# Optimization experiments

Measured on AMD Instinct MI355X. Metric: run time of the kernel, lower is better.

## Reference

```python
import jax, jax.numpy as jnp
import numpy as np

B, F, Q, CHUNK = 2, 8192, 4096, 512
NUM_VERTS = 6000


def _safe_div(n, d):
    return n / jnp.where(d == 0, 1.0, d)


def _bary(a, b, c, p):
    """Barycentric coords of the closest point on triangle (a,b,c) to p.
    All args broadcastable [..., 3]; returns [..., 3] (u, v, w) with
    closest = u*a + v*b + w*c. Ericson, Real-Time Collision Detection."""
    ab = b - a; ac = c - a; ap = p - a
    d1 = jnp.sum(ab * ap, -1); d2 = jnp.sum(ac * ap, -1)
    bp = p - b
    d3 = jnp.sum(ab * bp, -1); d4 = jnp.sum(ac * bp, -1)
    cp_ = p - c
    d5 = jnp.sum(ab * cp_, -1); d6 = jnp.sum(ac * cp_, -1)
    vc = d1 * d4 - d3 * d2
    vb = d5 * d2 - d1 * d6
    va = d3 * d6 - d5 * d4
    v_ab = _safe_div(d1, d1 - d3)
    w_ac = _safe_div(d2, d2 - d6)
    w_bc = _safe_div(d4 - d3, (d4 - d3) + (d5 - d6))
    inv = _safe_div(1.0, va + vb + vc)
    v_in = vb * inv; w_in = vc * inv
    zero = jnp.zeros_like(d1); one = jnp.ones_like(d1)
    conds = [(d1 <= 0) & (d2 <= 0),
             (d3 >= 0) & (d4 <= d3),
             (vc <= 0) & (d1 >= 0) & (d3 <= 0),
             (d6 >= 0) & (d5 <= d6),
             (vb <= 0) & (d2 >= 0) & (d6 <= 0),
             (va <= 0) & (d4 >= d3) & (d5 >= d6)]
    u = jnp.select(conds, [one, zero, 1 - v_ab, zero, 1 - w_ac, zero], 1 - v_in - w_in)
    v = jnp.select(conds, [zero, one, v_ab, zero, zero, 1 - w_bc], v_in)
    w = jnp.select(conds, [zero, zero, zero, one, w_ac, w_bc], w_in)
    return jnp.stack([u, v, w], -1)


def _closest_faces(triangles, points, chunk=CHUNK):
    """Exact closest-triangle index per query point (replaces BVH search).
    triangles [B,F,3,3], points [B,Q,3] -> int32 [B,Q]."""
    tri = jax.lax.stop_gradient(triangles)
    pts = jax.lax.stop_gradient(points)
    bsz, nq = pts.shape[0], pts.shape[1]
    a = tri[:, :, 0]; b = tri[:, :, 1]; c = tri[:, :, 2]  # [B,F,3]

    def one_chunk(p_chunk):  # [B,CH,3]
        pa = p_chunk[:, :, None, :]                       # [B,CH,1,3]
        bc = _bary(a[:, None], b[:, None], c[:, None], pa)  # [B,CH,F,3]
        cp = (bc[..., 0:1] * a[:, None] + bc[..., 1:2] * b[:, None]
              + bc[..., 2:3] * c[:, None])                # [B,CH,F,3]
        d2 = jnp.sum((cp - pa) ** 2, -1)                  # [B,CH,F]
        return jnp.argmin(d2, axis=-1)                    # [B,CH]

    chunks = jnp.moveaxis(pts.reshape(bsz, nq // chunk, chunk, 3), 1, 0)
    idx = jax.lax.map(one_chunk, chunks)                  # [NC,B,CH]
    return jnp.moveaxis(idx, 0, 1).reshape(bsz, nq)


def setup_inputs() -> dict:
    key = jax.random.key(0)
    k1, k2, k3, k4, k5 = jax.random.split(key, 5)
    return {
        'triangles': jax.random.normal(k1, (B, F, 3, 3), dtype=jnp.float32),
        'points': jax.random.normal(k2, (B, Q, 3), dtype=jnp.float32),
        'normals': jax.random.normal(k3, (B, F, 3, 3), dtype=jnp.float32),
        'cmaps': jax.random.normal(k4, (B, F, 3, 3), dtype=jnp.float32),
        'faces': jax.random.randint(k5, (B, F, 3), 0, NUM_VERTS, dtype=jnp.int32),
    }


def reference(triangles, points, normals, cmaps, faces):
    closest_faces = _closest_faces(triangles, points)     # [B,Q]
    idx = closest_faces[:, :, None, None]
    tri_g = jnp.take_along_axis(triangles, idx, axis=1)   # [B,Q,3,3]
    nrm_g = jnp.take_along_axis(normals, idx, axis=1)
    cmp_g = jnp.take_along_axis(cmaps, idx, axis=1)
    bcs = _bary(tri_g[:, :, 0], tri_g[:, :, 1], tri_g[:, :, 2], points)  # [B,Q,3]
    bcs = jnp.clip(bcs, 0.0, 1.0)
    closest_points = jnp.einsum('bqk,bqkd->bqd', bcs, tri_g)
    closest_normals = jnp.einsum('bqk,bqkd->bqd', bcs, nrm_g)
    closest_cmaps = jnp.einsum('bqk,bqkd->bqd', bcs, cmp_g)
    residual = closest_points - points
    closest_fids = jnp.take_along_axis(faces, closest_faces[:, :, None], axis=1)  # [B,Q,3]
    closest_idx = jnp.take_along_axis(
        closest_fids, jnp.argmax(bcs, -1)[:, :, None], axis=2)[..., 0]            # [B,Q]
    return residual, closest_normals, closest_cmaps, closest_idx
```

## Files before the change

### kernel.cpp

```cpp
#include <hip/hip_runtime.h>
#include <float.h>

#define B_   2
#define F_   8192
#define Q_   4096
#define NC   128
#define FC   (F_/NC)
#define PTS  512
#define PPT  2

typedef float f4u __attribute__((ext_vector_type(4), aligned(4)));
typedef float f2u __attribute__((ext_vector_type(2), aligned(8)));
typedef unsigned int uint;

__device__ __forceinline__ void bary_uvw(
    float ax, float ay, float az,
    float bx, float by, float bz,
    float cx, float cy, float cz,
    float px, float py, float pz,
    float& u, float& v, float& w)
{
#pragma clang fp contract(off)
    float abx = bx - ax, aby = by - ay, abz = bz - az;
    float acx = cx - ax, acy = cy - ay, acz = cz - az;
    float apx = px - ax, apy = py - ay, apz = pz - az;
    float d1 = abx*apx + aby*apy + abz*apz;
    float d2 = acx*apx + acy*apy + acz*apz;
    float bpx = px - bx, bpy = py - by, bpz = pz - bz;
    float d3 = abx*bpx + aby*bpy + abz*bpz;
    float d4 = acx*bpx + acy*bpy + acz*bpz;
    float qx = px - cx, qy = py - cy, qz = pz - cz;
    float d5 = abx*qx + aby*qy + abz*qz;
    float d6 = acx*qx + acy*qy + acz*qz;
    float vc = d1*d4 - d3*d2;
    float vb = d5*d2 - d1*d6;
    float va = d3*d6 - d5*d4;

    bool c1 = (d1 <= 0.f) && (d2 <= 0.f);
    bool c2 = (d3 >= 0.f) && (d4 <= d3);
    bool c3 = (vc <= 0.f) && (d1 >= 0.f) && (d3 <= 0.f);
    bool c4 = (d6 >= 0.f) && (d5 <= d6);
    bool c5 = (vb <= 0.f) && (d2 >= 0.f) && (d6 <= 0.f);
    bool c6 = (va <= 0.f) && (d4 >= d3) && (d5 >= d6);

    bool e1 = c1;
    bool p1 = !c1;
    bool e2 = p1 && c2;
    bool p2 = p1 && !c2;
    bool e3 = p2 && c3;
    bool p3 = p2 && !c3;
    bool e4 = p3 && c4;
    bool p4 = p3 && !c4;
    bool e5 = p4 && c5;
    bool p5 = p4 && !c5;
    bool e6 = p5 && c6;

    float d43 = d4 - d3;
    float d56 = d5 - d6;
    float n  = e3 ? d1        : (e5 ? d2        : (e6 ? d43         : 1.f));
    float dd = e3 ? (d1 - d3) : (e5 ? (d2 - d6) : (e6 ? (d43 + d56) : (va + vb + vc)));
    dd = (dd == 0.f) ? 1.f : dd;
    float t = n / dd;

    float vi = vb * t;
    float wi = vc * t;
    u = e1 ? 1.f : (e2 ? 0.f : (e3 ? 1.f - t : (e4 ? 0.f : (e5 ? 1.f - t : (e6 ? 0.f     : 1.f - vi - wi)))));
    v = e1 ? 0.f : (e2 ? 1.f : (e3 ? t       : (e4 ? 0.f : (e5 ? 0.f     : (e6 ? 1.f - t : vi)))));
    w = e1 ? 0.f : (e2 ? 0.f : (e3 ? 0.f     : (e4 ? 1.f : (e5 ? t       : (e6 ? t       : wi)))));
}

__global__ void precompute_kernel(const float* __restrict__ tri,
                                  float4* __restrict__ cons)
{
    int i = blockIdx.x * blockDim.x + threadIdx.x;
    if (i >= B_ * F_) return;
    const float* g = tri + (size_t)i * 9;
    float ax = g[0], ay = g[1], az = g[2];
    float bx = g[3], by = g[4], bz = g[5];
    float cx = g[6], cy = g[7], cz = g[8];
    float abx = bx - ax, aby = by - ay, abz = bz - az;
    float acx = cx - ax, acy = cy - ay, acz = cz - az;
    float daa = abx*abx + aby*aby + abz*abz;
    float dcc = acx*acx + acy*acy + acz*acz;
    float dac = abx*acx + aby*acy + abz*acz;
    float dbc = daa + dcc - 2.f*dac;
    float nn  = daa*dcc - dac*dac;
    float4* o = cons + (size_t)i * 6;
    o[0] = make_float4(abx, aby, abz, -(abx*ax + aby*ay + abz*az));
    o[1] = make_float4(acx, acy, acz, -(acx*ax + acy*ay + acz*az));
    o[2] = make_float4(-2.f*ax, -2.f*ay, -2.f*az, ax*ax + ay*ay + az*az);
    o[3] = make_float4(daa, dcc, -dac, nn);
    o[4] = make_float4(1.f/daa, 1.f/dcc, 1.f/dbc, 1.f/nn);
    o[5] = make_float4(daa - dac, -daa, -dcc, -dbc);
}

__device__ __forceinline__ void eval_key(
    float px, float py, float pz, float pp,
    const f4u C0, const f4u C1, const f4u C2, const f4u C3, const f4u C4,
    const f4u C5, int flv, int im, int& K0, int& K1)
{
    float d1, d2, ap, ins, sg, t1, t2, ts;
    asm("v_mov_b32 %[d1], %[nabA]\n\t"
        "v_mov_b32 %[d2], %[nacA]\n\t"
        "v_mov_b32 %[ap], %[aa]\n\t"
        "v_fmac_f32 %[d1], %[abx], %[px]\n\t"
        "v_fmac_f32 %[d2], %[acx], %[px]\n\t"
        "v_fmac_f32 %[ap], %[n2ax], %[px]\n\t"
        "v_fmac_f32 %[d1], %[aby], %[py]\n\t"
        "v_fmac_f32 %[d2], %[acy], %[py]\n\t"
        "v_fmac_f32 %[ap], %[n2ay], %[py]\n\t"
        "v_fmac_f32 %[d1], %[abz], %[pz]\n\t"
        "v_fmac_f32 %[d2], %[acz], %[pz]\n\t"
        "v_fmac_f32 %[ap], %[n2az], %[pz]\n\t"
        "v_mul_f32 %[t1], %[dcc], %[d1]\n\t"
        "v_mul_f32 %[t2], %[daa], %[d2]\n\t"
        "v_add_f32 %[ap], %[pp], %[ap]\n\t"
        "v_fmac_f32 %[t1], %[ndac], %[d2]\n\t"
        "v_fmac_f32 %[t2], %[ndac], %[d1]\n\t"
        "v_add_f32 %[ts], %[t1], %[t2]\n\t"
        "v_mul_f32 %[sg], %[d1], %[t1]\n\t"
        "v_sub_f32 %[ts], %[nn], %[ts]\n\t"
        "v_fmac_f32 %[sg], %[d2], %[t2]\n\t"
        "v_min3_f32 %[ins], %[t1], %[t2], %[ts]\n\t"
        "v_mul_f32 %[sg], %[rnn], %[sg]"
        : [d1]"=&v"(d1), [d2]"=&v"(d2), [ap]"=&v"(ap), [ins]"=&v"(ins),
          [sg]"=&v"(sg), [t1]"=&v"(t1), [t2]"=&v"(t2), [ts]"=&v"(ts)
        : [px]"v"(px), [py]"v"(py), [pz]"v"(pz), [pp]"v"(pp),
          [abx]"s"(C0.x), [aby]"s"(C0.y), [abz]"s"(C0.z), [nabA]"s"(C0.w),
          [acx]"s"(C1.x), [acy]"s"(C1.y), [acz]"s"(C1.z), [nacA]"s"(C1.w),
          [n2ax]"s"(C2.x), [n2ay]"s"(C2.y), [n2az]"s"(C2.z), [aa]"s"(C2.w),
          [daa]"s"(C3.x), [dcc]"s"(C3.y), [ndac]"s"(C3.z), [nn]"s"(C3.w),
          [rnn]"s"(C4.w));

    float ta, tc, t3, t4, t5, t7, t8;
    unsigned long long mk;
    asm("v_mul_f32 %[ta], %[rdaa], %[d1]\n\t"
        "v_mul_f32 %[tc], %[rdcc], %[d2]\n\t"
        "v_sub_f32 %[t7], %[d2], %[d1]\n\t"
        "v_med3_f32 %[ta], %[ta], 0, 1.0\n\t"
        "v_med3_f32 %[tc], %[tc], 0, 1.0\n\t"
        "v_add_f32 %[t7], %[kk], %[t7]\n\t"
        "v_add_f32 %[t3], %[d1], %[d1]\n\t"
        "v_add_f32 %[t4], %[d2], %[d2]\n\t"
        "v_mul_f32 %[t8], %[rdbc], %[t7]\n\t"
        "v_fma_f32 %[t5], %[ndaa], %[ta], %[t3]\n\t"
        "v_fma_f32 %[t4], %[ndcc], %[tc], %[t4]\n\t"
        "v_med3_f32 %[t8], %[t8], 0, 1.0\n\t"
        "v_add_f32 %[t7], %[t7], %[t7]\n\t"
        "v_mul_f32 %[ta], %[ta], %[t5]\n\t"
        "v_mul_f32 %[tc], %[tc], %[t4]\n\t"
        "v_fma_f32 %[t7], %[ndbc], %[t8], %[t7]\n\t"
        "v_subrev_f32 %[t3], %[daa], %[t3]\n\t"
        "v_mul_f32 %[t7], %[t8], %[t7]\n\t"
        "v_cmp_le_f32 %[mk], 0, %[ins]\n\t"
        "v_add_f32 %[t7], %[t3], %[t7]\n\t"
        "v_max3_f32 %[t3], %[ta], %[tc], %[t7]\n\t"
        "v_cndmask_b32 %[t3], %[t3], %[sg], %[mk]\n\t"
        "v_sub_f32 %[t4], %[ap], %[t3]\n\t"
        "v_and_or_b32 %[t4], %[t4], %[im], %[flv]\n\t"
        "v_max_i32 %[t8], %[K0], %[t4]\n\t"
        "v_min_i32 %[K0], %[K0], %[t4]\n\t"
        "v_min_i32 %[K1], %[K1], %[t8]"
        : [K0]"+v"(K0), [K1]"+v"(K1),
          [ta]"=&v"(ta), [tc]"=&v"(tc), [t3]"=&v"(t3), [t4]"=&v"(t4),
          [t5]"=&v"(t5), [t7]"=&v"(t7), [t8]"=&v"(t8), [mk]"=&s"(mk)
        : [d1]"v"(d1), [d2]"v"(d2), [ins]"v"(ins), [sg]"v"(sg), [ap]"v"(ap),
          [daa]"s"(C3.x), [rdaa]"s"(C4.x), [rdcc]"s"(C4.y), [rdbc]"s"(C4.z),
          [kk]"s"(C5.x), [ndaa]"s"(C5.y), [ndcc]"s"(C5.z), [ndbc]"s"(C5.w),
          [im]"s"(im), [flv]"v"(flv));
}

__global__ __launch_bounds__(PTS, 8) void scan_kernel(
    const float* __restrict__ tri, const float* __restrict__ pts,
    const f4u* __restrict__ cons, uint2* __restrict__ keys)
{
    const int im = ~(FC - 1);
    const int tid = threadIdx.x;
    const int pb = blockIdx.x, cb = blockIdx.y, bb = blockIdx.z;

    const int q0 = pb * (PTS * PPT) + tid * PPT;
    const float* p0 = pts + ((size_t)bb * Q_ + q0) * 3;
    f2u m0 = *(const f2u*)(p0);
    f2u m1 = *(const f2u*)(p0 + 2);
    f2u m2 = *(const f2u*)(p0 + 4);
    float px0 = m0.x, py0 = m0.y, pz0 = m1.x;
    float px1 = m1.y, py1 = m2.x, pz1 = m2.y;
    float pp0 = px0*px0 + py0*py0 + pz0*pz0;
    float pp1 = px1*px1 + py1*py1 + pz1*pz1;

    const f4u* ct = cons + ((size_t)bb * F_ + (size_t)cb * FC) * 6;

    int K00 = 0x7FFFFFFF, K01 = 0x7FFFFFFF;
    int K10 = 0x7FFFFFFF, K11 = 0x7FFFFFFF;

    f4u A0 = ct[0], A1 = ct[1], A2 = ct[2], A3 = ct[3], A4 = ct[4], A5 = ct[5];
    #pragma unroll 2
    for (int fl = 0; fl < FC; ++fl) {
        int nf = (fl + 1 < FC) ? fl + 1 : FC - 1;
        const f4u* nt = ct + nf * 6;
        f4u N0 = nt[0], N1 = nt[1], N2 = nt[2], N3 = nt[3], N4 = nt[4], N5 = nt[5];
        eval_key(px0, py0, pz0, pp0, A0, A1, A2, A3, A4, A5, fl, im, K00, K01);
        eval_key(px1, py1, pz1, pp1, A0, A1, A2, A3, A4, A5, fl, im, K10, K11);
        A0 = N0; A1 = N1; A2 = N2; A3 = N3; A4 = N4; A5 = N5;
    }

    float pxs[2] = {px0, px1};
    float pys[2] = {py0, py1};
    float pzs[2] = {pz0, pz1};
    int kk0[2] = {K00, K10};
    int kk1[2] = {K01, K11};

    #pragma unroll
    for (int p = 0; p < 2; ++p) {
        float px = pxs[p], py = pys[p], pz = pzs[p];
        float dbest = FLT_MAX; int fbest = 0x7FFFFFFF;
        #pragma unroll
        for (int j = 0; j < 2; ++j) {
            int lf = (j == 0 ? kk0[p] : kk1[p]) & (FC - 1);
            const float* tg = tri + ((size_t)bb * F_ + (size_t)cb * FC + lf) * 9;
            f4u ra4 = *(const f4u*)(tg);
            f4u rb4 = *(const f4u*)(tg + 4);
            float rc8 = tg[8];
            float u, v, w;
            bary_uvw(ra4.x, ra4.y, ra4.z, ra4.w, rb4.x, rb4.y,
                     rb4.z, rb4.w, rc8, px, py, pz, u, v, w);
            float d2v;
            {
#pragma clang fp contract(off)
                float cpx = u*ra4.x + v*ra4.w + w*rb4.z;
                float cpy = u*ra4.y + v*rb4.x + w*rb4.w;
                float cpz = u*ra4.z + v*rb4.y + w*rc8;
                float dx = cpx - px, dy = cpy - py, dz = cpz - pz;
                d2v = dx*dx + dy*dy + dz*dz;
            }
            int face = cb * FC + lf;
            if (d2v < dbest || (d2v == dbest && face < fbest)) { dbest = d2v; fbest = face; }
        }
        keys[((size_t)bb * Q_ + q0 + p) * NC + cb] = make_uint2(__float_as_uint(dbest), (uint)fbest);
    }
}

__global__ __launch_bounds__(256) void finalize_kernel(
    const float* __restrict__ tri, const float* __restrict__ pts,
    const float* __restrict__ nrm, const float* __restrict__ cmp,
    const int* __restrict__ faces,
    const uint2* __restrict__ keys,
    float* __restrict__ out)
{
#pragma clang fp contract(off)
    const int lane = threadIdx.x & 63;
    const int t = blockIdx.x * 4 + (threadIdx.x >> 6);
    const int bb = t >> 12;

    uint4 K = ((const uint4*)keys)[(size_t)t * (NC/2) + lane];
    float dbest = __uint_as_float(K.x); int fbest = (int)K.y;
    float d1v   = __uint_as_float(K.z); int f1v   = (int)K.w;
    if (d1v < dbest || (d1v == dbest && f1v < fbest)) { dbest = d1v; fbest = f1v; }
    for (int off = 32; off > 0; off >>= 1) {
        float od = __shfl_down(dbest, off);
        int   of = __shfl_down(fbest, off);
        if (od < dbest || (od == dbest && of < fbest)) { dbest = od; fbest = of; }
    }
    if (lane != 0) return;

    const float* pp = pts + (size_t)t * 3;
    float px = pp[0], py = pp[1], pz = pp[2];

    const int bestf = fbest;
    const float* tg = tri + ((size_t)bb * F_ + bestf) * 9;
    const float* ng = nrm + ((size_t)bb * F_ + bestf) * 9;
    const float* cg = cmp + ((size_t)bb * F_ + bestf) * 9;
    f4u TA = *(const f4u*)(tg), TB = *(const f4u*)(tg + 4);
    float TC = tg[8];
    f4u NA = *(const f4u*)(ng), NB = *(const f4u*)(ng + 4);
    float NCs = ng[8];
    f4u CA = *(const f4u*)(cg), CB = *(const f4u*)(cg + 4);
    float CC = cg[8];

    float u, v, w;
    bary_uvw(TA.x, TA.y, TA.z, TA.w, TB.x, TB.y, TB.z, TB.w, TC,
             px, py, pz, u, v, w);
    u = fminf(fmaxf(u, 0.f), 1.f);
    v = fminf(fmaxf(v, 0.f), 1.f);
    w = fminf(fmaxf(w, 0.f), 1.f);

    float cpx = u * TA.x + v * TA.w + w * TB.z;
    float cpy = u * TA.y + v * TB.x + w * TB.w;
    float cpz = u * TA.z + v * TB.y + w * TC;
    float nx  = u * NA.x + v * NA.w + w * NB.z;
    float ny  = u * NA.y + v * NB.x + w * NB.w;
    float nz  = u * NA.z + v * NB.y + w * NCs;
    float mx  = u * CA.x + v * CA.w + w * CB.z;
    float my  = u * CA.y + v * CB.x + w * CB.w;
    float mz  = u * CA.z + v * CB.y + w * CC;

    const size_t S3 = (size_t)B_ * Q_ * 3;
    out[(size_t)t * 3 + 0] = cpx - px;
    out[(size_t)t * 3 + 1] = cpy - py;
    out[(size_t)t * 3 + 2] = cpz - pz;
    out[S3 + (size_t)t * 3 + 0] = nx;
    out[S3 + (size_t)t * 3 + 1] = ny;
    out[S3 + (size_t)t * 3 + 2] = nz;
    out[2 * S3 + (size_t)t * 3 + 0] = mx;
    out[2 * S3 + (size_t)t * 3 + 1] = my;
    out[2 * S3 + (size_t)t * 3 + 2] = mz;

    int k = 0; float mm = u;
    if (v > mm) { mm = v; k = 1; }
    if (w > mm) { k = 2; }
    out[3 * S3 + t] = (float)faces[((size_t)bb * F_ + bestf) * 3 + k];
}

extern "C" void kernel_launch(void* const* d_in, const int* in_sizes, int n_in,
                              void* d_out, int out_size, void* d_ws, size_t ws_size,
                              hipStream_t stream) {
    const float* tri   = (const float*)d_in[0];
    const float* pts   = (const float*)d_in[1];
    const float* nrm   = (const float*)d_in[2];
    const float* cmp   = (const float*)d_in[3];
    const int*   faces = (const int*)d_in[4];
    float* out = (float*)d_out;

    uint2*  keys = (uint2*)d_ws;
    float4* cons = (float4*)((char*)d_ws + (size_t)B_ * Q_ * NC * sizeof(uint2));

    precompute_kernel<<<(B_ * F_ + 255) / 256, 256, 0, stream>>>(tri, cons);

    dim3 g1(Q_ / (PTS * PPT), NC, B_);
    scan_kernel<<<g1, PTS, 0, stream>>>(tri, pts, (const f4u*)cons, keys);
    finalize_kernel<<<(B_ * Q_) / 4, 256, 0, stream>>>(
        tri, pts, nrm, cmp, faces, keys, out);
}
```

Measured before the change: 145.1 us.

## Use packed FP32 math over face pairs with interleaved constant layout

Precomputed per-face constants are now stored interleaved for pairs of faces, so each uniform load yields two faces' values as a packed pair. The front half of the key evaluation uses v_pk_fma/v_pk_mul to process two faces per instruction. The back half stays scalar per face. Launch bounds drop from 8 to 4 waves per SIMD to allow more registers. The aim is fewer VALU issue slots per face, at the cost of a different rounding order (separate mul then add for the constant term) and possibly lower occupancy.

```diff
diff --git a/kernel.cpp b/kernel.cpp
--- a/kernel.cpp
+++ b/kernel.cpp
@@ -11,6 +11,7 @@
 
 typedef float f4u __attribute__((ext_vector_type(4), aligned(4)));
 typedef float f2u __attribute__((ext_vector_type(2), aligned(8)));
+typedef float f2  __attribute__((ext_vector_type(2)));
 typedef unsigned int uint;
 
 __device__ __forceinline__ void bary_uvw(
@@ -70,7 +71,7 @@
 }
 
 __global__ void precompute_kernel(const float* __restrict__ tri,
-                                  float4* __restrict__ cons)
+                                  float* __restrict__ consf)
 {
     int i = blockIdx.x * blockDim.x + threadIdx.x;
     if (i >= B_ * F_) return;
@@ -85,56 +86,68 @@
     float dac = abx*acx + aby*acy + abz*acz;
     float dbc = daa + dcc - 2.f*dac;
     float nn  = daa*dcc - dac*dac;
-    float4* o = cons + (size_t)i * 6;
-    o[0] = make_float4(abx, aby, abz, -(abx*ax + aby*ay + abz*az));
-    o[1] = make_float4(acx, acy, acz, -(acx*ax + acy*ay + acz*az));
-    o[2] = make_float4(-2.f*ax, -2.f*ay, -2.f*az, ax*ax + ay*ay + az*az);
-    o[3] = make_float4(daa, dcc, -dac, nn);
-    o[4] = make_float4(1.f/daa, 1.f/dcc, 1.f/dbc, 1.f/nn);
-    o[5] = make_float4(daa - dac, -daa, -dcc, -dbc);
-}
-
-__device__ __forceinline__ void eval_key(
-    float px, float py, float pz, float pp,
-    const f4u C0, const f4u C1, const f4u C2, const f4u C3, const f4u C4,
-    const f4u C5, int flv, int im, int& K0, int& K1)
-{
-    float d1, d2, ap, ins, sg, t1, t2, ts;
-    asm("v_mov_b32 %[d1], %[nabA]\n\t"
-        "v_mov_b32 %[d2], %[nacA]\n\t"
-        "v_mov_b32 %[ap], %[aa]\n\t"
-        "v_fmac_f32 %[d1], %[abx], %[px]\n\t"
-        "v_fmac_f32 %[d2], %[acx], %[px]\n\t"
-        "v_fmac_f32 %[ap], %[n2ax], %[px]\n\t"
-        "v_fmac_f32 %[d1], %[aby], %[py]\n\t"
-        "v_fmac_f32 %[d2], %[acy], %[py]\n\t"
-        "v_fmac_f32 %[ap], %[n2ay], %[py]\n\t"
-        "v_fmac_f32 %[d1], %[abz], %[pz]\n\t"
-        "v_fmac_f32 %[d2], %[acz], %[pz]\n\t"
-        "v_fmac_f32 %[ap], %[n2az], %[pz]\n\t"
-        "v_mul_f32 %[t1], %[dcc], %[d1]\n\t"
-        "v_mul_f32 %[t2], %[daa], %[d2]\n\t"
-        "v_add_f32 %[ap], %[pp], %[ap]\n\t"
-        "v_fmac_f32 %[t1], %[ndac], %[d2]\n\t"
-        "v_fmac_f32 %[t2], %[ndac], %[d1]\n\t"
-        "v_add_f32 %[ts], %[t1], %[t2]\n\t"
-        "v_mul_f32 %[sg], %[d1], %[t1]\n\t"
-        "v_sub_f32 %[ts], %[nn], %[ts]\n\t"
-        "v_fmac_f32 %[sg], %[d2], %[t2]\n\t"
-        "v_min3_f32 %[ins], %[t1], %[t2], %[ts]\n\t"
-        "v_mul_f32 %[sg], %[rnn], %[sg]"
-        : [d1]"=&v"(d1), [d2]"=&v"(d2), [ap]"=&v"(ap), [ins]"=&v"(ins),
-          [sg]"=&v"(sg), [t1]"=&v"(t1), [t2]"=&v"(t2), [ts]"=&v"(ts)
-        : [px]"v"(px), [py]"v"(py), [pz]"v"(pz), [pp]"v"(pp),
-          [abx]"s"(C0.x), [aby]"s"(C0.y), [abz]"s"(C0.z), [nabA]"s"(C0.w),
-          [acx]"s"(C1.x), [acy]"s"(C1.y), [acz]"s"(C1.z), [nacA]"s"(C1.w),
-          [n2ax]"s"(C2.x), [n2ay]"s"(C2.y), [n2az]"s"(C2.z), [aa]"s"(C2.w),
-          [daa]"s"(C3.x), [dcc]"s"(C3.y), [ndac]"s"(C3.z), [nn]"s"(C3.w),
-          [rnn]"s"(C4.w));
-
-    float ta, tc, t3, t4, t5, t7, t8;
+    float* o = consf + (size_t)(i >> 1) * 48 + (i & 1);
+    o[0]  = abx;  o[2]  = aby;  o[4]  = abz;  o[6]  = -(abx*ax + aby*ay + abz*az);
+    o[8]  = acx;  o[10] = acy;  o[12] = acz;  o[14] = -(acx*ax + acy*ay + acz*az);
+    o[16] = -2.f*ax; o[18] = -2.f*ay; o[20] = -2.f*az; o[22] = ax*ax + ay*ay + az*az;
+    o[24] = daa;  o[26] = dcc;  o[28] = -dac; o[30] = nn;
+    o[32] = 1.f/daa; o[34] = 1.f/dcc; o[36] = 1.f/dbc; o[38] = 1.f/nn;
+    o[40] = daa - dac; o[42] = -daa; o[44] = -dcc; o[46] = -dbc;
+}
+
+__device__ __forceinline__ void eval_front(
+    f2 pxx, f2 pyy, f2 pzz, f2 ppp, f2 neg1,
+    f2 abx, f2 aby, f2 abz, f2 nabA,
+    f2 acx, f2 acy, f2 acz, f2 nacA,
+    f2 n2ax, f2 n2ay, f2 n2az, f2 aa,
+    f2 daa, f2 dcc, f2 ndac, f2 nn, f2 rnn,
+    f2& d1o, f2& d2o, f2& apo, f2& t1o, f2& t2o, f2& tso, f2& sgo)
+{
+    f2 d1, d2, ap, t1, t2, ts, sg;
+    asm("v_pk_mul_f32 %[d1], %[abx], %[pxx]\n\t"
+        "v_pk_mul_f32 %[d2], %[acx], %[pxx]\n\t"
+        "v_pk_mul_f32 %[ap], %[n2ax], %[pxx]\n\t"
+        "v_pk_fma_f32 %[d1], %[aby], %[pyy], %[d1]\n\t"
+        "v_pk_fma_f32 %[d2], %[acy], %[pyy], %[d2]\n\t"
+        "v_pk_fma_f32 %[ap], %[n2ay], %[pyy], %[ap]\n\t"
+        "v_pk_fma_f32 %[d1], %[abz], %[pzz], %[d1]\n\t"
+        "v_pk_fma_f32 %[d2], %[acz], %[pzz], %[d2]\n\t"
+        "v_pk_fma_f32 %[ap], %[n2az], %[pzz], %[ap]\n\t"
+        "v_pk_add_f32 %[d1], %[nabA], %[d1]\n\t"
+        "v_pk_add_f32 %[d2], %[nacA], %[d2]\n\t"
+        "v_pk_add_f32 %[ap], %[aa], %[ap]\n\t"
+        "v_pk_mul_f32 %[t1], %[dcc], %[d1]\n\t"
+        "v_pk_mul_f32 %[t2], %[daa], %[d2]\n\t"
+        "v_pk_add_f32 %[ap], %[ppp], %[ap]\n\t"
+        "v_pk_fma_f32 %[t1], %[ndac], %[d2], %[t1]\n\t"
+        "v_pk_fma_f32 %[t2], %[ndac], %[d1], %[t2]\n\t"
+        "v_pk_add_f32 %[ts], %[t1], %[t2]\n\t"
+        "v_pk_mul_f32 %[sg], %[t1], %[d1]\n\t"
+        "v_pk_fma_f32 %[ts], %[ts], %[neg1], %[nn]\n\t"
+        "v_pk_fma_f32 %[sg], %[t2], %[d2], %[sg]\n\t"
+        "v_pk_mul_f32 %[sg], %[rnn], %[sg]"
+        : [d1]"=&v"(d1), [d2]"=&v"(d2), [ap]"=&v"(ap), [t1]"=&v"(t1),
+          [t2]"=&v"(t2), [ts]"=&v"(ts), [sg]"=&v"(sg)
+        : [pxx]"v"(pxx), [pyy]"v"(pyy), [pzz]"v"(pzz), [ppp]"v"(ppp),
+          [neg1]"v"(neg1),
+          [abx]"s"(abx), [aby]"s"(aby), [abz]"s"(abz), [nabA]"s"(nabA),
+          [acx]"s"(acx), [acy]"s"(acy), [acz]"s"(acz), [nacA]"s"(nacA),
+          [n2ax]"s"(n2ax), [n2ay]"s"(n2ay), [n2az]"s"(n2az), [aa]"s"(aa),
+          [daa]"s"(daa), [dcc]"s"(dcc), [ndac]"s"(ndac), [nn]"s"(nn),
+          [rnn]"s"(rnn));
+    d1o = d1; d2o = d2; apo = ap; t1o = t1; t2o = t2; tso = ts; sgo = sg;
+}
+
+__device__ __forceinline__ void eval_back(
+    float d1, float d2, float t1, float t2, float ts, float sg, float ap,
+    float daa, float rdaa, float rdcc, float rdbc,
+    float kk, float ndaa, float ndcc, float ndbc,
+    int flv, int im, int& K0, int& K1)
+{
+    float ta, tc, t3, t4, t5, t7, t8, ins;
     unsigned long long mk;
-    asm("v_mul_f32 %[ta], %[rdaa], %[d1]\n\t"
+    asm("v_min3_f32 %[ins], %[t1], %[t2], %[ts]\n\t"
+        "v_mul_f32 %[ta], %[rdaa], %[d1]\n\t"
         "v_mul_f32 %[tc], %[rdcc], %[d2]\n\t"
         "v_sub_f32 %[t7], %[d2], %[d1]\n\t"
         "v_med3_f32 %[ta], %[ta], 0, 1.0\n\t"
@@ -163,16 +176,18 @@
         "v_min_i32 %[K1], %[K1], %[t8]"
         : [K0]"+v"(K0), [K1]"+v"(K1),
           [ta]"=&v"(ta), [tc]"=&v"(tc), [t3]"=&v"(t3), [t4]"=&v"(t4),
-          [t5]"=&v"(t5), [t7]"=&v"(t7), [t8]"=&v"(t8), [mk]"=&s"(mk)
-        : [d1]"v"(d1), [d2]"v"(d2), [ins]"v"(ins), [sg]"v"(sg), [ap]"v"(ap),
-          [daa]"s"(C3.x), [rdaa]"s"(C4.x), [rdcc]"s"(C4.y), [rdbc]"s"(C4.z),
-          [kk]"s"(C5.x), [ndaa]"s"(C5.y), [ndcc]"s"(C5.z), [ndbc]"s"(C5.w),
+          [t5]"=&v"(t5), [t7]"=&v"(t7), [t8]"=&v"(t8), [ins]"=&v"(ins),
+          [mk]"=&s"(mk)
+        : [d1]"v"(d1), [d2]"v"(d2), [t1]"v"(t1), [t2]"v"(t2), [ts]"v"(ts),
+          [sg]"v"(sg), [ap]"v"(ap),
+          [daa]"s"(daa), [rdaa]"s"(rdaa), [rdcc]"s"(rdcc), [rdbc]"s"(rdbc),
+          [kk]"s"(kk), [ndaa]"s"(ndaa), [ndcc]"s"(ndcc), [ndbc]"s"(ndbc),
           [im]"s"(im), [flv]"v"(flv));
 }
 
-__global__ __launch_bounds__(PTS, 8) void scan_kernel(
+__global__ __launch_bounds__(PTS, 4) void scan_kernel(
     const float* __restrict__ tri, const float* __restrict__ pts,
-    const f4u* __restrict__ cons, uint2* __restrict__ keys)
+    const float* __restrict__ consf, uint2* __restrict__ keys)
 {
     const int im = ~(FC - 1);
     const int tid = threadIdx.x;
@@ -188,20 +203,53 @@
     float pp0 = px0*px0 + py0*py0 + pz0*pz0;
     float pp1 = px1*px1 + py1*py1 + pz1*pz1;
 
-    const f4u* ct = cons + ((size_t)bb * F_ + (size_t)cb * FC) * 6;
+    f2 PX0 = {px0, px0}, PY0 = {py0, py0}, PZ0 = {pz0, pz0}, PP0 = {pp0, pp0};
+    f2 PX1 = {px1, px1}, PY1 = {py1, py1}, PZ1 = {pz1, pz1}, PP1 = {pp1, pp1};
+    f2 NEG1 = {-1.f, -1.f};
+
+    const float* ctf = consf + (size_t)((bb * F_ + cb * FC) >> 1) * 48;
 
     int K00 = 0x7FFFFFFF, K01 = 0x7FFFFFFF;
     int K10 = 0x7FFFFFFF, K11 = 0x7FFFFFFF;
 
-    f4u A0 = ct[0], A1 = ct[1], A2 = ct[2], A3 = ct[3], A4 = ct[4], A5 = ct[5];
     #pragma unroll 2
-    for (int fl = 0; fl < FC; ++fl) {
-        int nf = (fl + 1 < FC) ? fl + 1 : FC - 1;
-        const f4u* nt = ct + nf * 6;
-        f4u N0 = nt[0], N1 = nt[1], N2 = nt[2], N3 = nt[3], N4 = nt[4], N5 = nt[5];
-        eval_key(px0, py0, pz0, pp0, A0, A1, A2, A3, A4, A5, fl, im, K00, K01);
-        eval_key(px1, py1, pz1, pp1, A0, A1, A2, A3, A4, A5, fl, im, K10, K11);
-        A0 = N0; A1 = N1; A2 = N2; A3 = N3; A4 = N4; A5 = N5;
+    for (int j = 0; j < FC/2; ++j) {
+        const f4u* cr = (const f4u*)ctf + j * 12;
+        f4u r0 = cr[0], r1 = cr[1], r2 = cr[2],  r3 = cr[3];
+        f4u r4 = cr[4], r5 = cr[5], r6 = cr[6],  r7 = cr[7];
+        f4u r8 = cr[8], r9 = cr[9], r10 = cr[10], r11 = cr[11];
+        f2 abx = {r0.x, r0.y},  aby = {r0.z, r0.w};
+        f2 abz = {r1.x, r1.y},  nabA = {r1.z, r1.w};
+        f2 acx = {r2.x, r2.y},  acy = {r2.z, r2.w};
+        f2 acz = {r3.x, r3.y},  nacA = {r3.z, r3.w};
+        f2 n2ax = {r4.x, r4.y}, n2ay = {r4.z, r4.w};
+        f2 n2az = {r5.x, r5.y}, aa = {r5.z, r5.w};
+        f2 daa = {r6.x, r6.y},  dcc = {r6.z, r6.w};
+        f2 ndac = {r7.x, r7.y}, nn = {r7.z, r7.w};
+        f2 rnn = {r9.z, r9.w};
+
+        int fl0 = 2*j, fl1 = 2*j + 1;
+        f2 d1, d2, ap, t1, t2, ts, sg;
+
+        eval_front(PX0, PY0, PZ0, PP0, NEG1, abx, aby, abz, nabA,
+                   acx, acy, acz, nacA, n2ax, n2ay, n2az, aa,
+                   daa, dcc, ndac, nn, rnn, d1, d2, ap, t1, t2, ts, sg);
+        eval_back(d1.x, d2.x, t1.x, t2.x, ts.x, sg.x, ap.x,
+                  r6.x, r8.x, r8.z, r9.x, r10.x, r10.z, r11.x, r11.z,
+                  fl0, im, K00, K01);
+        eval_back(d1.y, d2.y, t1.y, t2.y, ts.y, sg.y, ap.y,
+                  r6.y, r8.y, r8.w, r9.y, r10.y, r10.w, r11.y, r11.w,
+                  fl1, im, K00, K01);
+
+        eval_front(PX1, PY1, PZ1, PP1, NEG1, abx, aby, abz, nabA,
+                   acx, acy, acz, nacA, n2ax, n2ay, n2az, aa,
+                   daa, dcc, ndac, nn, rnn, d1, d2, ap, t1, t2, ts, sg);
+        eval_back(d1.x, d2.x, t1.x, t2.x, ts.x, sg.x, ap.x,
+                  r6.x, r8.x, r8.z, r9.x, r10.x, r10.z, r11.x, r11.z,
+                  fl0, im, K10, K11);
+        eval_back(d1.y, d2.y, t1.y, t2.y, ts.y, sg.y, ap.y,
+                  r6.y, r8.y, r8.w, r9.y, r10.y, r10.w, r11.y, r11.w,
+                  fl1, im, K10, K11);
     }
 
     float pxs[2] = {px0, px1};
@@ -321,13 +369,13 @@
     const int*   faces = (const int*)d_in[4];
     float* out = (float*)d_out;
 
-    uint2*  keys = (uint2*)d_ws;
-    float4* cons = (float4*)((char*)d_ws + (size_t)B_ * Q_ * NC * sizeof(uint2));
-
-    precompute_kernel<<<(B_ * F_ + 255) / 256, 256, 0, stream>>>(tri, cons);
+    uint2* keys = (uint2*)d_ws;
+    float* consf = (float*)((char*)d_ws + (size_t)B_ * Q_ * NC * sizeof(uint2));
+
+    precompute_kernel<<<(B_ * F_ + 255) / 256, 256, 0, stream>>>(tri, consf);
 
     dim3 g1(Q_ / (PTS * PPT), NC, B_);
-    scan_kernel<<<g1, PTS, 0, stream>>>(tri, pts, (const f4u*)cons, keys);
+    scan_kernel<<<g1, PTS, 0, stream>>>(tri, pts, consf, keys);
     finalize_kernel<<<(B_ * Q_) / 4, 256, 0, stream>>>(
         tri, pts, nrm, cmp, faces, keys, out);
 }
```

Result: slower. 149.7 us (+3.1%).

## Replace per-chunk key buffer and reduction with 64-bit atomicMin table

Applied to the files above, without the earlier changes.

Instead of writing one (distance, face) pair per face chunk to a large key buffer and reducing 128 entries per query in the finalize kernel, each scan thread packs distance and face index into a 64-bit key and does atomicMin into a per-query table initialized in the precompute kernel. The epilogue then reads one key per query with one thread each. This removes the 8 MB key buffer traffic and the wave-shuffle reduction, at the cost of global atomic contention (128 atomics per query). The packing relies on non-negative float bits ordering like unsigned ints, which gives the same smallest-distance-then-lowest-face tiebreak.

```diff
diff --git a/kernel.cpp b/kernel.cpp
--- a/kernel.cpp
+++ b/kernel.cpp
@@ -12,6 +12,7 @@
 typedef float f4u __attribute__((ext_vector_type(4), aligned(4)));
 typedef float f2u __attribute__((ext_vector_type(2), aligned(8)));
 typedef unsigned int uint;
+typedef unsigned long long u64;
 
 __device__ __forceinline__ void bary_uvw(
     float ax, float ay, float az,
@@ -70,10 +71,12 @@
 }
 
 __global__ void precompute_kernel(const float* __restrict__ tri,
-                                  float4* __restrict__ cons)
+                                  float4* __restrict__ cons,
+                                  u64* __restrict__ tbl)
 {
     int i = blockIdx.x * blockDim.x + threadIdx.x;
     if (i >= B_ * F_) return;
+    if (i < B_ * Q_) tbl[i] = ~0ull;
     const float* g = tri + (size_t)i * 9;
     float ax = g[0], ay = g[1], az = g[2];
     float bx = g[3], by = g[4], bz = g[5];
@@ -172,7 +175,7 @@
 
 __global__ __launch_bounds__(PTS, 8) void scan_kernel(
     const float* __restrict__ tri, const float* __restrict__ pts,
-    const f4u* __restrict__ cons, uint2* __restrict__ keys)
+    const f4u* __restrict__ cons, u64* __restrict__ tbl)
 {
     const int im = ~(FC - 1);
     const int tid = threadIdx.x;
@@ -236,37 +239,28 @@
             int face = cb * FC + lf;
             if (d2v < dbest || (d2v == dbest && face < fbest)) { dbest = d2v; fbest = face; }
         }
-        keys[((size_t)bb * Q_ + q0 + p) * NC + cb] = make_uint2(__float_as_uint(dbest), (uint)fbest);
+        u64 pk = ((u64)(uint)__float_as_uint(dbest) << 32) | (uint)fbest;
+        atomicMin(&tbl[(size_t)bb * Q_ + q0 + p], pk);
     }
 }
 
-__global__ __launch_bounds__(256) void finalize_kernel(
+__global__ void epilogue_kernel(
     const float* __restrict__ tri, const float* __restrict__ pts,
     const float* __restrict__ nrm, const float* __restrict__ cmp,
     const int* __restrict__ faces,
-    const uint2* __restrict__ keys,
+    const u64* __restrict__ tbl,
     float* __restrict__ out)
 {
 #pragma clang fp contract(off)
-    const int lane = threadIdx.x & 63;
-    const int t = blockIdx.x * 4 + (threadIdx.x >> 6);
+    const int t = blockIdx.x * blockDim.x + threadIdx.x;
+    if (t >= B_ * Q_) return;
     const int bb = t >> 12;
 
-    uint4 K = ((const uint4*)keys)[(size_t)t * (NC/2) + lane];
-    float dbest = __uint_as_float(K.x); int fbest = (int)K.y;
-    float d1v   = __uint_as_float(K.z); int f1v   = (int)K.w;
-    if (d1v < dbest || (d1v == dbest && f1v < fbest)) { dbest = d1v; fbest = f1v; }
-    for (int off = 32; off > 0; off >>= 1) {
-        float od = __shfl_down(dbest, off);
-        int   of = __shfl_down(fbest, off);
-        if (od < dbest || (od == dbest && of < fbest)) { dbest = od; fbest = of; }
-    }
-    if (lane != 0) return;
+    const int bestf = (int)(uint)(tbl[t] & 0xFFFFFFFFu);
 
     const float* pp = pts + (size_t)t * 3;
     float px = pp[0], py = pp[1], pz = pp[2];
 
-    const int bestf = fbest;
     const float* tg = tri + ((size_t)bb * F_ + bestf) * 9;
     const float* ng = nrm + ((size_t)bb * F_ + bestf) * 9;
     const float* cg = cmp + ((size_t)bb * F_ + bestf) * 9;
@@ -321,13 +315,14 @@
     const int*   faces = (const int*)d_in[4];
     float* out = (float*)d_out;
 
-    uint2*  keys = (uint2*)d_ws;
-    float4* cons = (float4*)((char*)d_ws + (size_t)B_ * Q_ * NC * sizeof(uint2));
-
-    precompute_kernel<<<(B_ * F_ + 255) / 256, 256, 0, stream>>>(tri, cons);
+    u64*    tbl  = (u64*)d_ws;
+    float4* cons = (float4*)((char*)d_ws + (size_t)B_ * Q_ * sizeof(u64));
+
+    precompute_kernel<<<(B_ * F_ + 255) / 256, 256, 0, stream>>>(tri, cons, tbl);
 
     dim3 g1(Q_ / (PTS * PPT), NC, B_);
-    scan_kernel<<<g1, PTS, 0, stream>>>(tri, pts, (const f4u*)cons, keys);
-    finalize_kernel<<<(B_ * Q_) / 4, 256, 0, stream>>>(
-        tri, pts, nrm, cmp, faces, keys, out);
-}
+    scan_kernel<<<g1, PTS, 0, stream>>>(tri, pts, (const f4u*)cons, tbl);
+
+    epilogue_kernel<<<(B_ * Q_ + 255) / 256, 256, 0, stream>>>(
+        tri, pts, nrm, cmp, faces, tbl, out);
+}
```

Result: faster. 139.8 us (-3.7%).
